# Kernel optimization log

Measured on AMD Instinct MI355X. Metric: run time of the kernel, lower is better.

## Reference

```python
import jax, jax.numpy as jnp
import numpy as np

B, G, K = 16, 5000, 256
NUM_CELLS, HID = 100, 64
STEPS, ALPHA = 10, 0.1


def setup_inputs() -> dict:
    key = jax.random.key(0)
    ks = jax.random.split(key, 10)
    ctl = jax.random.normal(ks[0], (B, G), dtype=jnp.float32)
    drug_targets = jax.random.uniform(ks[1], (B, G), dtype=jnp.float32)
    cell_idx = jax.random.randint(ks[2], (B,), 0, NUM_CELLS)
    drug_fp = jax.random.normal(ks[3], (B, 128), dtype=jnp.float32)
    # gene->module membership matrix (constructor constant M_gk)
    M = jax.random.uniform(ks[4], (G, K), dtype=jnp.float32)
    # module-module adjacency (constructor constant A_kk), column-normalized for stability
    A = jax.random.uniform(ks[5], (K, K), dtype=jnp.float32)
    A = A / jnp.sum(A, axis=0, keepdims=True)
    # shared Dense(hidden_dim, relu): input feature dim is 3 (ctl, t, z_gene stacked)
    W1 = jax.random.normal(ks[6], (3, HID), dtype=jnp.float32) * 0.5
    b1 = jnp.zeros((HID,), dtype=jnp.float32)
    cell_emb = jax.random.normal(ks[7], (NUM_CELLS, HID), dtype=jnp.float32) * 0.05
    W2 = jax.random.normal(ks[8], (HID, 1), dtype=jnp.float32) * 0.1
    b2 = jnp.zeros((1,), dtype=jnp.float32)
    return {"ctl": ctl, "drug_targets": drug_targets, "cell_idx": cell_idx,
            "drug_fp": drug_fp, "M": M, "A": A, "W1": W1, "b1": b1,
            "cell_emb": cell_emb, "W2": W2, "b2": b2}


def reference(ctl, drug_targets, cell_idx, drug_fp, M, A, W1, b1, cell_emb, W2, b2):
    t = drug_targets                                   # [B, G]
    # max-pool gene targets into modules: max_g t[b,g] * M[g,k]
    t_mod = jnp.max(t[:, :, None] * M[None, :, :], axis=1)   # [B, K]
    # APPNP propagation: Z = (1-alpha) * Z @ A + alpha * S, fixed 10 steps
    Z = t_mod
    for _ in range(STEPS):
        Z = (1.0 - ALPHA) * (Z @ A) + ALPHA * t_mod
    z_gene = Z @ M.T                                   # [B, G]
    x = jnp.stack([ctl, t, z_gene], axis=-1)           # [B, G, 3]
    h = jax.nn.relu(x @ W1 + b1)                       # [B, G, HID]
    h = h + cell_emb[cell_idx][:, None, :]             # broadcast cell embedding
    y = jnp.squeeze(h @ W2 + b2, axis=-1)              # [B, G]
    return y
```

## Files before the change

kernel.cpp:

```cpp
#include <hip/hip_runtime.h>

#define G 5000
#define K 256
#define BATCH 16
#define HID 64
#define STEPS 10
#define NC 125
#define GPER 40

__global__ __launch_bounds__(256)
void maxpool_kernel(const float* __restrict__ t,
                    const float* __restrict__ M,
                    const float* __restrict__ A,
                    float* __restrict__ partials,
                    float* __restrict__ awarm) {
    __shared__ float tl[GPER][BATCH];
    const int c   = blockIdx.x >> 1;
    const int kh  = blockIdx.x & 1;
    const int tid = threadIdx.x;
    const int kl  = tid & 127;
    const int bg  = tid >> 7;
    const int g0  = c * GPER;
    const int k   = kh * 128 + kl;

    float4 aw = make_float4(0.f, 0.f, 0.f, 0.f);
    if (tid < 64)
        aw = ((const float4*)A)[((size_t)blockIdx.x * 64 + tid) & 16383];

    for (int i = tid; i < GPER * BATCH; i += 256) {
        int gi = i >> 4, b = i & 15;
        tl[gi][b] = t[b * G + g0 + gi];
    }
    __syncthreads();

    float mrow[GPER];
#pragma unroll
    for (int gi = 0; gi < GPER; ++gi)
        mrow[gi] = M[(size_t)(g0 + gi) * K + k];

    float mx[8];
#pragma unroll
    for (int b = 0; b < 8; ++b) mx[b] = 0.f;

#pragma unroll
    for (int gi = 0; gi < GPER; ++gi) {
#pragma unroll
        for (int b = 0; b < 8; ++b)
            mx[b] = fmaxf(mx[b], tl[gi][bg * 8 + b] * mrow[gi]);
    }
#pragma unroll
    for (int b = 0; b < 8; ++b)
        partials[((size_t)c * BATCH + bg * 8 + b) * K + k] = mx[b];

    if (tid < 64) awarm[tid] = aw.x + aw.y + aw.z + aw.w;
}

__global__ __launch_bounds__(1024, 4)
void appnp_fused(const float* __restrict__ partials,
                 const float* __restrict__ A,
                 const int* __restrict__ cell_idx,
                 const float* __restrict__ cell_emb,
                 const float* __restrict__ W2,
                 const float* __restrict__ b2,
                 float* __restrict__ Zfin,
                 float* __restrict__ ce_dot) {
    __shared__ float4 zb[2][K / 4];
    __shared__ float  Sm[K];
    __shared__ float  red[16][K];
    __shared__ float  ce_red[HID];

    const int b  = blockIdx.x;
    const int t  = threadIdx.x;
    const int k  = t & 255;
    const int jc = t >> 8;
    const int j0 = jc * 64;

    float Areg[64];
#pragma unroll
    for (int jj = 0; jj < 64; ++jj)
        Areg[jj] = A[(size_t)(j0 + jj) * K + k];

    {
        const int k4 = t & 63;
        const int cg = t >> 6;
        const float4* p4 = (const float4*)partials;
        float4 m4 = make_float4(0.f, 0.f, 0.f, 0.f);
        for (int c = cg; c < NC; c += 16) {
            float4 v = p4[((size_t)c * BATCH + b) * (K / 4) + k4];
            m4.x = fmaxf(m4.x, v.x);
            m4.y = fmaxf(m4.y, v.y);
            m4.z = fmaxf(m4.z, v.z);
            m4.w = fmaxf(m4.w, v.w);
        }
        ((float4*)red[cg])[k4] = m4;
    }
    if (t < HID) {
        int ci = cell_idx[b];
        ce_red[t] = cell_emb[ci * HID + t] * W2[t];
    }
    __syncthreads();
    if (jc == 0) {
        float s = red[0][k];
#pragma unroll
        for (int cgi = 1; cgi < 16; ++cgi) s = fmaxf(s, red[cgi][k]);
        Sm[k] = s;
        ((float*)zb)[k] = s;
    }
    if (t == 0) {
        float s = b2[0];
        for (int h = 0; h < HID; ++h) s += ce_red[h];
        ce_dot[b] = s;
    }
    __syncthreads();

    for (int s = 0; s < STEPS; ++s) {
        const float4* cur4 = zb[s & 1] + (j0 >> 2);
        float*        nxt  = (float*)zb[(s + 1) & 1];
        float acc = 0.f;
#pragma unroll
        for (int q = 0; q < 16; ++q) {
            float4 c4 = cur4[q];
            acc = fmaf(c4.x, Areg[4 * q + 0], acc);
            acc = fmaf(c4.y, Areg[4 * q + 1], acc);
            acc = fmaf(c4.z, Areg[4 * q + 2], acc);
            acc = fmaf(c4.w, Areg[4 * q + 3], acc);
        }
        red[jc][k] = acc;
        __syncthreads();
        if (jc == 0)
            nxt[k] = 0.9f * (red[0][k] + red[1][k] + red[2][k] + red[3][k])
                   + 0.1f * Sm[k];
        __syncthreads();
    }
    if (jc == 0) Zfin[b * K + k] = ((float*)zb)[k];
}

__global__ __launch_bounds__(256)
void final_kernel(const float* __restrict__ ctl,
                  const float* __restrict__ t_in,
                  const float* __restrict__ Z,
                  const float* __restrict__ M,
                  const float* __restrict__ W1,
                  const float* __restrict__ b1,
                  const float* __restrict__ W2,
                  const float* __restrict__ ce_dot,
                  float* __restrict__ out) {
    __shared__ float4 zl[8 * (K / 4)];
    __shared__ float4 wpack[HID];
    __shared__ float  w2l[HID];
    __shared__ float  cel[8];

    const int tid = threadIdx.x;
    const int bh  = blockIdx.x & 1;
    const int gb  = blockIdx.x >> 1;
    const int b0  = bh * 8;

    const float4* Z4 = (const float4*)Z + (size_t)b0 * (K / 4);
    for (int i = tid; i < 8 * (K / 4); i += 256) zl[i] = Z4[i];
    if (tid < HID) {
        wpack[tid] = make_float4(W1[tid], W1[HID + tid], W1[2 * HID + tid], b1[tid]);
        w2l[tid] = W2[tid];
    }
    if (tid < 8) cel[tid] = ce_dot[b0 + tid];
    __syncthreads();

    const int gl = tid & 63;
    const int bg = tid >> 6;
    const int g  = gb * 64 + gl;
    if (g >= G) return;

    const float4* M4 = (const float4*)(M + (size_t)g * K);

    float acc0 = 0.f, acc1 = 0.f;
    float4 mc[8];
#pragma unroll
    for (int u = 0; u < 8; ++u) mc[u] = M4[u];

#pragma unroll
    for (int kc = 0; kc < 8; ++kc) {
        float4 mn[8];
        if (kc < 7) {
#pragma unroll
            for (int u = 0; u < 8; ++u) mn[u] = M4[(kc + 1) * 8 + u];
        }
#pragma unroll
        for (int u = 0; u < 8; ++u) {
            const int k4 = kc * 8 + u;
            float4 m4 = mc[u];
            float4 za = zl[(bg * 2 + 0) * (K / 4) + k4];
            float4 zc = zl[(bg * 2 + 1) * (K / 4) + k4];
            acc0 = fmaf(m4.x, za.x, acc0);
            acc0 = fmaf(m4.y, za.y, acc0);
            acc0 = fmaf(m4.z, za.z, acc0);
            acc0 = fmaf(m4.w, za.w, acc0);
            acc1 = fmaf(m4.x, zc.x, acc1);
            acc1 = fmaf(m4.y, zc.y, acc1);
            acc1 = fmaf(m4.z, zc.z, acc1);
            acc1 = fmaf(m4.w, zc.w, acc1);
        }
        if (kc < 7) {
#pragma unroll
            for (int u = 0; u < 8; ++u) mc[u] = mn[u];
        }
    }

    const int ba = b0 + bg * 2;
    const int bb = ba + 1;
    float cva = ctl[ba * G + g], cvb = ctl[bb * G + g];
    float tva = t_in[ba * G + g], tvb = t_in[bb * G + g];
    float ya  = cel[bg * 2],      yb  = cel[bg * 2 + 1];
#pragma unroll 8
    for (int h = 0; h < HID; ++h) {
        float4 w = wpack[h];
        float w2h = w2l[h];
        float pa = fmaf(cva, w.x, fmaf(tva, w.y, fmaf(acc0, w.z, w.w)));
        pa = fmaxf(pa, 0.f);
        ya = fmaf(pa, w2h, ya);
        float pb = fmaf(cvb, w.x, fmaf(tvb, w.y, fmaf(acc1, w.z, w.w)));
        pb = fmaxf(pb, 0.f);
        yb = fmaf(pb, w2h, yb);
    }
    out[ba * G + g] = ya;
    out[bb * G + g] = yb;
}

extern "C" void kernel_launch(void* const* d_in, const int* in_sizes, int n_in,
                              void* d_out, int out_size, void* d_ws, size_t ws_size,
                              hipStream_t stream) {
    const float* ctl      = (const float*)d_in[0];
    const float* tgt      = (const float*)d_in[1];
    const int*   cell_idx = (const int*)d_in[2];
    const float* M        = (const float*)d_in[4];
    const float* A        = (const float*)d_in[5];
    const float* W1       = (const float*)d_in[6];
    const float* b1       = (const float*)d_in[7];
    const float* cell_emb = (const float*)d_in[8];
    const float* W2       = (const float*)d_in[9];
    const float* b2       = (const float*)d_in[10];
    float* out = (float*)d_out;

    float* partials = (float*)d_ws;
    float* Zfin  = partials + (size_t)NC * BATCH * K;
    float* ce    = Zfin + BATCH * K;
    float* awarm = ce + BATCH;

    maxpool_kernel<<<NC * 2, 256, 0, stream>>>(tgt, M, A, partials, awarm);
    appnp_fused<<<BATCH, 1024, 0, stream>>>(partials, A, cell_idx, cell_emb,
                                            W2, b2, Zfin, ce);
    final_kernel<<<79 * 2, 256, 0, stream>>>(ctl, tgt, Zfin, M, W1, b1,
                                             W2, ce, out);
}
```

Measured before the change: 107.2 us.

## Restructure APPNP block to 512 threads with 4-wide output register tiles

The propagation kernel now runs 512 threads per batch row instead of 1024. Each thread holds a 32x4 tile of A in float4 registers and computes four output modules per step, so every loaded Z value feeds four FMAs and the A loads are vectorized. The cross-warp reduction is split 8 ways over all 256 rows, and the seed vector stays in a register rather than shared memory. In exchange each thread carries more register pressure and there are fewer waves to hide latency across the serial 10-step loop.

```diff
diff --git a/kernel.cpp b/kernel.cpp
--- a/kernel.cpp
+++ b/kernel.cpp
@@ -55,7 +55,7 @@
     if (tid < 64) awarm[tid] = aw.x + aw.y + aw.z + aw.w;
 }
 
-__global__ __launch_bounds__(1024, 4)
+__global__ __launch_bounds__(512, 2)
 void appnp_fused(const float* __restrict__ partials,
                  const float* __restrict__ A,
                  const int* __restrict__ cell_idx,
@@ -64,47 +64,50 @@
                  const float* __restrict__ b2,
                  float* __restrict__ Zfin,
                  float* __restrict__ ce_dot) {
-    __shared__ float4 zb[2][K / 4];
-    __shared__ float  Sm[K];
-    __shared__ float  red[16][K];
+    __shared__ float4 zb4[2][K / 4];
+    __shared__ float4 red4[8][K / 4];
     __shared__ float  ce_red[HID];
 
     const int b  = blockIdx.x;
     const int t  = threadIdx.x;
-    const int k  = t & 255;
-    const int jc = t >> 8;
-    const int j0 = jc * 64;
-
-    float Areg[64];
-#pragma unroll
-    for (int jj = 0; jj < 64; ++jj)
-        Areg[jj] = A[(size_t)(j0 + jj) * K + k];
+    const int l  = t & 63;
+    const int w  = t >> 6;
+    const int j0 = w * 32;
+    const int k0 = l * 4;
+
+    float4 Areg[32];
+#pragma unroll
+    for (int jj = 0; jj < 32; ++jj)
+        Areg[jj] = *(const float4*)&A[(size_t)(j0 + jj) * K + k0];
 
     {
         const int k4 = t & 63;
         const int cg = t >> 6;
         const float4* p4 = (const float4*)partials;
         float4 m4 = make_float4(0.f, 0.f, 0.f, 0.f);
-        for (int c = cg; c < NC; c += 16) {
+        for (int c = cg; c < NC; c += 8) {
             float4 v = p4[((size_t)c * BATCH + b) * (K / 4) + k4];
             m4.x = fmaxf(m4.x, v.x);
             m4.y = fmaxf(m4.y, v.y);
             m4.z = fmaxf(m4.z, v.z);
             m4.w = fmaxf(m4.w, v.w);
         }
-        ((float4*)red[cg])[k4] = m4;
+        red4[cg][k4] = m4;
     }
     if (t < HID) {
         int ci = cell_idx[b];
         ce_red[t] = cell_emb[ci * HID + t] * W2[t];
     }
     __syncthreads();
-    if (jc == 0) {
-        float s = red[0][k];
-#pragma unroll
-        for (int cgi = 1; cgi < 16; ++cgi) s = fmaxf(s, red[cgi][k]);
-        Sm[k] = s;
-        ((float*)zb)[k] = s;
+
+    float Smreg = 0.f;
+    const float* red = (const float*)red4;
+    if (t < K) {
+        float s = red[t];
+#pragma unroll
+        for (int j = 1; j < 8; ++j) s = fmaxf(s, red[j * K + t]);
+        Smreg = s;
+        ((float*)zb4)[t] = s;
     }
     if (t == 0) {
         float s = b2[0];
@@ -114,25 +117,33 @@
     __syncthreads();
 
     for (int s = 0; s < STEPS; ++s) {
-        const float4* cur4 = zb[s & 1] + (j0 >> 2);
-        float*        nxt  = (float*)zb[(s + 1) & 1];
-        float acc = 0.f;
-#pragma unroll
-        for (int q = 0; q < 16; ++q) {
-            float4 c4 = cur4[q];
-            acc = fmaf(c4.x, Areg[4 * q + 0], acc);
-            acc = fmaf(c4.y, Areg[4 * q + 1], acc);
-            acc = fmaf(c4.z, Areg[4 * q + 2], acc);
-            acc = fmaf(c4.w, Areg[4 * q + 3], acc);
-        }
-        red[jc][k] = acc;
+        const float4* zc = zb4[s & 1] + w * 8;
+        float4 acc = make_float4(0.f, 0.f, 0.f, 0.f);
+#pragma unroll
+        for (int q = 0; q < 8; ++q) {
+            float4 z4 = zc[q];
+            float4 A0 = Areg[4 * q + 0], A1 = Areg[4 * q + 1];
+            float4 A2 = Areg[4 * q + 2], A3 = Areg[4 * q + 3];
+            acc.x = fmaf(z4.x, A0.x, acc.x); acc.x = fmaf(z4.y, A1.x, acc.x);
+            acc.x = fmaf(z4.z, A2.x, acc.x); acc.x = fmaf(z4.w, A3.x, acc.x);
+            acc.y = fmaf(z4.x, A0.y, acc.y); acc.y = fmaf(z4.y, A1.y, acc.y);
+            acc.y = fmaf(z4.z, A2.y, acc.y); acc.y = fmaf(z4.w, A3.y, acc.y);
+            acc.z = fmaf(z4.x, A0.z, acc.z); acc.z = fmaf(z4.y, A1.z, acc.z);
+            acc.z = fmaf(z4.z, A2.z, acc.z); acc.z = fmaf(z4.w, A3.z, acc.z);
+            acc.w = fmaf(z4.x, A0.w, acc.w); acc.w = fmaf(z4.y, A1.w, acc.w);
+            acc.w = fmaf(z4.z, A2.w, acc.w); acc.w = fmaf(z4.w, A3.w, acc.w);
+        }
+        red4[w][l] = acc;
         __syncthreads();
-        if (jc == 0)
-            nxt[k] = 0.9f * (red[0][k] + red[1][k] + red[2][k] + red[3][k])
-                   + 0.1f * Sm[k];
+        if (t < K) {
+            float sum = red[t]         + red[K + t]     + red[2 * K + t]
+                      + red[3 * K + t] + red[4 * K + t] + red[5 * K + t]
+                      + red[6 * K + t] + red[7 * K + t];
+            ((float*)zb4)[((s + 1) & 1) * K + t] = fmaf(0.9f, sum, 0.1f * Smreg);
+        }
         __syncthreads();
     }
-    if (jc == 0) Zfin[b * K + k] = ((float*)zb)[k];
+    if (t < K) Zfin[b * K + t] = ((const float*)zb4)[t];
 }
 
 __global__ __launch_bounds__(256)
@@ -245,8 +256,8 @@
     float* awarm = ce + BATCH;
 
     maxpool_kernel<<<NC * 2, 256, 0, stream>>>(tgt, M, A, partials, awarm);
-    appnp_fused<<<BATCH, 1024, 0, stream>>>(partials, A, cell_idx, cell_emb,
-                                            W2, b2, Zfin, ce);
+    appnp_fused<<<BATCH, 512, 0, stream>>>(partials, A, cell_idx, cell_emb,
+                                           W2, b2, Zfin, ce);
     final_kernel<<<79 * 2, 256, 0, stream>>>(ctl, tgt, Zfin, M, W1, b1,
                                              W2, ce, out);
 }
```

After: 106.8 us. No clear change (-0.3%).
